# Optimization experiments

Measured on AMD Instinct MI355X. Metric: run time of the kernel, lower is better.

## Reference

```python
import jax, jax.numpy as jnp
import numpy as np

N = 50000        # num nodes
NFEAT = 512      # input feature dim
NCLASS = 256     # output classes (out_features of out_att)
E_RAND = 800000  # random edges; + N self-loops
NEG_SLOPE = 0.2  # leakyrelu alpha


def setup_inputs() -> dict:
    key = jax.random.key(0)
    k1, k2, k3, k4 = jax.random.split(key, 4)
    x = jax.random.normal(k1, (N, NFEAT), dtype=jnp.float32)
    W = jax.random.normal(k2, (NFEAT, NCLASS), dtype=jnp.float32) / np.float32(np.sqrt(NFEAT))
    a = jax.random.normal(k3, (2 * NCLASS,), dtype=jnp.float32) / np.float32(np.sqrt(2 * NCLASS))
    rand_edges = jax.random.randint(k4, (2, E_RAND), 0, N, dtype=jnp.int32)
    self_loops = jnp.tile(jnp.arange(N, dtype=jnp.int32), (2, 1))
    edge_index = jnp.concatenate([rand_edges, self_loops], axis=1)  # [2, E]
    return {"x": x, "W": W, "a": a, "edge_index": edge_index}


def reference(x, W, a, edge_index):
    # Eval-mode SpGAT: dropout is identity (training=False).
    row, col = edge_index[0], edge_index[1]  # edge = adj.nonzero().t(): row aggregates from col
    h = x @ W                                # [N, F]
    F_out = h.shape[1]
    # a @ cat(h[row], h[col]) == (h @ a1)[row] + (h @ a2)[col]  (avoids [E, 2F] concat)
    s_row = h @ a[:F_out]                    # [N]
    s_col = h @ a[F_out:]                    # [N]
    logits = s_row[row] + s_col[col]         # [E]
    e = jnp.exp(-jax.nn.leaky_relu(logits, negative_slope=NEG_SLOPE))  # [E]
    rowsum = jax.ops.segment_sum(e, row, num_segments=N)               # [N]
    msgs = e[:, None] * h[col]                                         # [E, F]
    h_prime = jax.ops.segment_sum(msgs, row, num_segments=N) / rowsum[:, None]
    return jax.nn.log_softmax(jax.nn.elu(h_prime), axis=1)
```

## Files before the change

### kernel.cpp

```cpp
#include <hip/hip_runtime.h>
#include <math.h>

#define NNODES   50000
#define NFEAT    512
#define NCLASS   256
#define NEG_SLOPE 0.2f
#define MPAD     50048
#define GBLK     782

typedef __attribute__((ext_vector_type(8))) short short8;
typedef __attribute__((ext_vector_type(4))) float floatx4;

__device__ __forceinline__ unsigned short f2bf(float f) {
    unsigned u = __builtin_bit_cast(unsigned, f);
    u += 0x7fffu + ((u >> 16) & 1u);
    return (unsigned short)(u >> 16);
}
__device__ __forceinline__ float bf2f(unsigned short s) {
    return __builtin_bit_cast(float, ((unsigned)s) << 16);
}
__device__ __forceinline__ float bf2f_lo(unsigned u) {
    return __builtin_bit_cast(float, u << 16);
}
__device__ __forceinline__ float bf2f_hi(unsigned u) {
    return __builtin_bit_cast(float, u & 0xffff0000u);
}
__device__ __forceinline__ unsigned pack_bf16_rh(float lo, float hi) {
    const unsigned ulo = __builtin_bit_cast(unsigned, lo) + 0x8000u;
    const unsigned uhi = __builtin_bit_cast(unsigned, hi) + 0x8000u;
    return __builtin_amdgcn_perm(uhi, ulo, 0x07060302);
}

#if __has_builtin(__builtin_amdgcn_fdot2_f32_bf16)
#define HAVE_DOT2 1
typedef __attribute__((ext_vector_type(2))) __bf16 bfx2;
__device__ __forceinline__ float dot2bf(unsigned hpair, unsigned epair, float acc) {
    return __builtin_amdgcn_fdot2_f32_bf16(__builtin_bit_cast(bfx2, hpair),
                                           __builtin_bit_cast(bfx2, epair), acc, false);
}
#endif

__global__ __launch_bounds__(256) void init_kernel(const float* __restrict__ W,
                                                   unsigned short* __restrict__ Wt,
                                                   int* __restrict__ zero2, int zn) {
    const int i = blockIdx.x * 256 + threadIdx.x;
    const int n = i >> 9;
    const int k = i & 511;
    Wt[i] = f2bf(W[(size_t)k * NCLASS + n]);
    for (int j = i; j < zn; j += 131072) zero2[j] = 0;
}

__global__ __launch_bounds__(256, 4) void gemm_mfma_kernel(const float* __restrict__ x,
                                                           const unsigned short* __restrict__ Wt,
                                                           unsigned short* __restrict__ hb,
                                                           const float* __restrict__ a,
                                                           float* __restrict__ s_row,
                                                           float* __restrict__ s_col,
                                                           const int* __restrict__ erow,
                                                           int* __restrict__ deg,
                                                           int M, int E) {
    __shared__ union {
        struct { short As[64 * 32]; short Bs[256 * 32]; } k;
        short Cs[32 * 260];
    } u;

    const int tid  = threadIdx.x;
    const int w    = tid >> 6;
    const int lane = tid & 63;
    const int rowbase = blockIdx.x * 64;

    const int srow = lane >> 2;
    const int skq  = (lane & 3) << 3;
    const int fm = lane & 15;
    const int fq = lane >> 4;

    floatx4 acc[4][4];
#pragma unroll
    for (int i = 0; i < 4; ++i)
#pragma unroll
        for (int j = 0; j < 4; ++j)
            acc[i][j] = (floatx4){0.f, 0.f, 0.f, 0.f};

    for (int k0 = 0; k0 < NFEAT; k0 += 32) {
#pragma unroll
        for (int t = 0; t < 4; ++t) {
            const int seg = w * 4 + t;
            const int nr  = seg * 16 + srow;
            __builtin_amdgcn_global_load_lds(
                (const __attribute__((address_space(1))) void*)(Wt + (size_t)nr * NFEAT + k0 + skq),
                (__attribute__((address_space(3))) void*)(u.k.Bs + seg * 512), 16, 0, 0);
        }
        {
            const int rr = w * 16 + srow;
            const int ar = min(rowbase + rr, M - 1);
            const float4* xp = (const float4*)&x[(size_t)ar * NFEAT + k0 + skq];
            const float4 u0 = xp[0];
            const float4 u1 = xp[1];
            uint4 o;
            o.x = pack_bf16_rh(u0.x, u0.y);
            o.y = pack_bf16_rh(u0.z, u0.w);
            o.z = pack_bf16_rh(u1.x, u1.y);
            o.w = pack_bf16_rh(u1.z, u1.w);
            *(uint4*)&u.k.As[rr * 32 + skq] = o;
        }
        __syncthreads();

        short8 af[4];
#pragma unroll
        for (int mt = 0; mt < 4; ++mt)
            af[mt] = *(const short8*)&u.k.As[(mt * 16 + fm) * 32 + fq * 8];
#pragma unroll
        for (int nt = 0; nt < 4; ++nt) {
            const short8 bfr = *(const short8*)&u.k.Bs[(w * 64 + nt * 16 + fm) * 32 + fq * 8];
#pragma unroll
            for (int mt = 0; mt < 4; ++mt)
                acc[mt][nt] = __builtin_amdgcn_mfma_f32_16x16x32_bf16(af[mt], bfr, acc[mt][nt], 0, 0, 0);
        }
        __syncthreads();
    }

#pragma unroll
    for (int p = 0; p < 2; ++p) {
        __syncthreads();
#pragma unroll
        for (int mt2 = 0; mt2 < 2; ++mt2) {
            const int mt = p * 2 + mt2;
#pragma unroll
            for (int nt = 0; nt < 4; ++nt)
#pragma unroll
                for (int r = 0; r < 4; ++r)
                    u.Cs[(mt2 * 16 + fq * 4 + r) * 260 + w * 64 + nt * 16 + fm] =
                        (short)f2bf(acc[mt][nt][r]);
        }
        __syncthreads();
#pragma unroll
        for (int k = 0; k < 8; ++k) {
            const int idx = tid + k * 256;
            const int lrow = idx >> 6;
            const int c4 = (idx & 63) << 2;
            const int grow = rowbase + p * 32 + lrow;
            const uint2 vv = *(const uint2*)&u.Cs[lrow * 260 + c4];
            const float f0 = bf2f_lo(vv.x), f1 = bf2f_hi(vv.x);
            const float f2 = bf2f_lo(vv.y), f3 = bf2f_hi(vv.y);
            const float4 A1 = *(const float4*)&a[c4];
            const float4 A2 = *(const float4*)&a[NCLASS + c4];
            float p1 = f0 * A1.x + f1 * A1.y + f2 * A1.z + f3 * A1.w;
            float p2 = f0 * A2.x + f1 * A2.y + f2 * A2.z + f3 * A2.w;
#pragma unroll
            for (int off = 1; off < 64; off <<= 1) {
                p1 += __shfl_xor(p1, off);
                p2 += __shfl_xor(p2, off);
            }
            if (grow < M) {
                *(uint2*)&hb[(size_t)grow * NCLASS + c4] = vv;
                if (lane == 0) {
                    s_row[grow] = p1;
                    s_col[grow] = p2;
                }
            }
        }
    }

    const int gtid = blockIdx.x * 256 + tid;
    for (int i = gtid; i < E; i += GBLK * 256)
        atomicAdd(&deg[erow[i]], 1);
}

__global__ __launch_bounds__(256) void scan1_kernel(const int* __restrict__ deg,
                                                    int* __restrict__ tmp,
                                                    int* __restrict__ blocksum, int n) {
    __shared__ int buf[256];
    const int i = blockIdx.x * 256 + threadIdx.x;
    const int t = threadIdx.x;
    buf[t] = (i < n) ? deg[i] : 0;
    __syncthreads();
#pragma unroll
    for (int off = 1; off < 256; off <<= 1) {
        const int uv = (t >= off) ? buf[t - off] : 0;
        __syncthreads();
        buf[t] += uv;
        __syncthreads();
    }
    if (i < n) tmp[i] = buf[t];
    if (t == 255) blocksum[blockIdx.x] = buf[255];
}

__global__ __launch_bounds__(256) void scan3_kernel(const int* __restrict__ tmp,
                                                    const int* __restrict__ blocksum,
                                                    int* __restrict__ rowstart, int n, int nb) {
    __shared__ int buf[256];
    const int t = threadIdx.x;
    buf[t] = (t < nb) ? blocksum[t] : 0;
    __syncthreads();
#pragma unroll
    for (int off = 1; off < 256; off <<= 1) {
        const int uv = (t >= off) ? buf[t - off] : 0;
        __syncthreads();
        buf[t] += uv;
        __syncthreads();
    }
    const int boff = (blockIdx.x == 0) ? 0 : buf[blockIdx.x - 1];
    const int i = blockIdx.x * 256 + t;
    if (i < n) rowstart[i + 1] = tmp[i] + boff;
    if (i == 0) rowstart[0] = 0;
}

__global__ __launch_bounds__(256) void scatter_kernel(const int* __restrict__ row,
                                                      const int* __restrict__ col,
                                                      const float* __restrict__ s_row,
                                                      const float* __restrict__ s_col,
                                                      const int* __restrict__ rowstart,
                                                      int* __restrict__ cursor,
                                                      int2* __restrict__ sorted_ce, int e) {
    const int i = blockIdx.x * 256 + threadIdx.x;
    if (i >= e) return;
    const int r = row[i];
    const int c = col[i];
    const float logit = s_row[r] + s_col[c];
    const float lr = logit > 0.f ? logit : NEG_SLOPE * logit;
    const float ew = __expf(-lr);
    const int pos = atomicAdd(&cursor[r], 1);
    int2 v;
    v.x = c;
    v.y = __builtin_bit_cast(int, ew);
    sorted_ce[rowstart[r] + pos] = v;
}

__global__ __launch_bounds__(256) void aggregate_kernel(const unsigned short* __restrict__ hb,
                                                        const int2* __restrict__ sorted_ce,
                                                        const int* __restrict__ rowstart,
                                                        float* __restrict__ out, int n) {
    const int wave = (int)((blockIdx.x * (size_t)blockDim.x + threadIdx.x) >> 6);
    const int lane = threadIdx.x & 63;
    if (wave >= n) return;
    const int r = wave;
    const int jb = rowstart[r];
    const int je = rowstart[r + 1];
    const int fo = lane << 2;

    float rowsum = 0.f;
    int j = jb;

#ifdef HAVE_DOT2
    float ac0 = 0.f, ac1 = 0.f, ac2 = 0.f, ac3 = 0.f;
    for (; j + 3 < je; j += 4) {
        const int2 v0 = sorted_ce[j];
        const int2 v1 = sorted_ce[j + 1];
        const int2 v2 = sorted_ce[j + 2];
        const int2 v3 = sorted_ce[j + 3];
        const uint2 g0 = *(const uint2*)&hb[(size_t)v0.x * NCLASS + fo];
        const uint2 g1 = *(const uint2*)&hb[(size_t)v1.x * NCLASS + fo];
        const uint2 g2 = *(const uint2*)&hb[(size_t)v2.x * NCLASS + fo];
        const uint2 g3 = *(const uint2*)&hb[(size_t)v3.x * NCLASS + fo];
        const float e0 = __builtin_bit_cast(float, v0.y);
        const float e1 = __builtin_bit_cast(float, v1.y);
        const float e2 = __builtin_bit_cast(float, v2.y);
        const float e3 = __builtin_bit_cast(float, v3.y);
        const unsigned ep01 = pack_bf16_rh(e0, e1);
        const unsigned ep23 = pack_bf16_rh(e2, e3);
        rowsum += (e0 + e1) + (e2 + e3);
        ac0 = dot2bf(__builtin_amdgcn_perm(g1.x, g0.x, 0x05040100), ep01, ac0);
        ac1 = dot2bf(__builtin_amdgcn_perm(g1.x, g0.x, 0x07060302), ep01, ac1);
        ac2 = dot2bf(__builtin_amdgcn_perm(g1.y, g0.y, 0x05040100), ep01, ac2);
        ac3 = dot2bf(__builtin_amdgcn_perm(g1.y, g0.y, 0x07060302), ep01, ac3);
        ac0 = dot2bf(__builtin_amdgcn_perm(g3.x, g2.x, 0x05040100), ep23, ac0);
        ac1 = dot2bf(__builtin_amdgcn_perm(g3.x, g2.x, 0x07060302), ep23, ac1);
        ac2 = dot2bf(__builtin_amdgcn_perm(g3.y, g2.y, 0x05040100), ep23, ac2);
        ac3 = dot2bf(__builtin_amdgcn_perm(g3.y, g2.y, 0x07060302), ep23, ac3);
    }
    float4 acc = make_float4(ac0, ac1, ac2, ac3);
#else
    float4 acc = make_float4(0.f, 0.f, 0.f, 0.f);
    for (; j + 3 < je; j += 4) {
        const int2 v0 = sorted_ce[j];
        const int2 v1 = sorted_ce[j + 1];
        const int2 v2 = sorted_ce[j + 2];
        const int2 v3 = sorted_ce[j + 3];
        const uint2 g0 = *(const uint2*)&hb[(size_t)v0.x * NCLASS + fo];
        const uint2 g1 = *(const uint2*)&hb[(size_t)v1.x * NCLASS + fo];
        const uint2 g2 = *(const uint2*)&hb[(size_t)v2.x * NCLASS + fo];
        const uint2 g3 = *(const uint2*)&hb[(size_t)v3.x * NCLASS + fo];
        const float e0 = __builtin_bit_cast(float, v0.y);
        const float e1 = __builtin_bit_cast(float, v1.y);
        const float e2 = __builtin_bit_cast(float, v2.y);
        const float e3 = __builtin_bit_cast(float, v3.y);
        rowsum += (e0 + e1) + (e2 + e3);
        acc.x += e0 * bf2f_lo(g0.x) + e1 * bf2f_lo(g1.x) + e2 * bf2f_lo(g2.x) + e3 * bf2f_lo(g3.x);
        acc.y += e0 * bf2f_hi(g0.x) + e1 * bf2f_hi(g1.x) + e2 * bf2f_hi(g2.x) + e3 * bf2f_hi(g3.x);
        acc.z += e0 * bf2f_lo(g0.y) + e1 * bf2f_lo(g1.y) + e2 * bf2f_lo(g2.y) + e3 * bf2f_lo(g3.y);
        acc.w += e0 * bf2f_hi(g0.y) + e1 * bf2f_hi(g1.y) + e2 * bf2f_hi(g2.y) + e3 * bf2f_hi(g3.y);
    }
#endif
    for (; j < je; ++j) {
        const int2 v = sorted_ce[j];
        const uint2 g = *(const uint2*)&hb[(size_t)v.x * NCLASS + fo];
        const float e = __builtin_bit_cast(float, v.y);
        rowsum += e;
        acc.x += e * bf2f_lo(g.x);
        acc.y += e * bf2f_hi(g.x);
        acc.z += e * bf2f_lo(g.y);
        acc.w += e * bf2f_hi(g.y);
    }

    const float inv = 1.f / rowsum;
    float v[4] = {acc.x * inv, acc.y * inv, acc.z * inv, acc.w * inv};
#pragma unroll
    for (int i = 0; i < 4; ++i)
        v[i] = v[i] > 0.f ? v[i] : __expf(v[i]) - 1.f;

    float m = fmaxf(fmaxf(v[0], v[1]), fmaxf(v[2], v[3]));
#pragma unroll
    for (int off = 32; off > 0; off >>= 1) m = fmaxf(m, __shfl_xor(m, off));
    float s = 0.f;
#pragma unroll
    for (int i = 0; i < 4; ++i) s += __expf(v[i] - m);
#pragma unroll
    for (int off = 32; off > 0; off >>= 1) s += __shfl_xor(s, off);
    const float lse = m + __logf(s);

    float4 o = make_float4(v[0] - lse, v[1] - lse, v[2] - lse, v[3] - lse);
    *(float4*)&out[(size_t)r * NCLASS + fo] = o;
}

extern "C" void kernel_launch(void* const* d_in, const int* in_sizes, int n_in,
                              void* d_out, int out_size, void* d_ws, size_t ws_size,
                              hipStream_t stream) {
    const float* x  = (const float*)d_in[0];
    const float* W  = (const float*)d_in[1];
    const float* a  = (const float*)d_in[2];
    const int* edge = (const int*)d_in[3];
    float* out = (float*)d_out;

    const int M = in_sizes[0] / NFEAT;
    const int E = in_sizes[3] / 2;
    const int* row = edge;
    const int* col = edge + E;

    char* ws = (char*)d_ws;
    size_t off = 0;
    auto carve = [&](size_t bytes) -> char* {
        char* p = ws + off;
        off = (off + bytes + 255) & ~(size_t)255;
        return p;
    };
    unsigned short* Wt = (unsigned short*)carve((size_t)NCLASS * NFEAT * sizeof(short));
    unsigned short* hb = (unsigned short*)carve((size_t)M * NCLASS * sizeof(short));
    int*   zero2    = (int*)carve((size_t)2 * M * sizeof(int));
    int*   deg      = zero2;
    int*   cursor   = zero2 + M;
    float* s_row    = (float*)carve((size_t)M * sizeof(float));
    float* s_col    = (float*)carve((size_t)M * sizeof(float));
    int*   rowstart = (int*)carve((size_t)(M + 1) * sizeof(int));
    int*   tmp_scan = (int*)carve((size_t)M * sizeof(int));
    int*   blocksum = (int*)carve((size_t)256 * sizeof(int));
    int2*  sorted_ce = (int2*)carve((size_t)E * sizeof(int2));

    init_kernel<<<512, 256, 0, stream>>>(W, Wt, zero2, 2 * M);

    gemm_mfma_kernel<<<GBLK, 256, 0, stream>>>(x, Wt, hb, a, s_row, s_col, row, deg, M, E);

    const int nb1 = (M + 255) / 256;
    scan1_kernel<<<nb1, 256, 0, stream>>>(deg, tmp_scan, blocksum, M);
    scan3_kernel<<<nb1, 256, 0, stream>>>(tmp_scan, blocksum, rowstart, M, nb1);
    scatter_kernel<<<(E + 255) / 256, 256, 0, stream>>>(row, col, s_row, s_col,
                                                        rowstart, cursor, sorted_ce, E);

    aggregate_kernel<<<(M + 3) / 4, 256, 0, stream>>>(hb, sorted_ce, rowstart, out, M);
}
```

Before: 328.2 us.

## Load GEMM fragments directly from global into registers with double buffering

The GEMM main loop no longer stages x and W tiles through LDS. Each lane loads its MFMA A and B fragments straight from global memory into registers, converting x to bf16 in registers, and prefetches the next k-step while the current MFMAs run. This drops both per-iteration __syncthreads and the LDS round trip. In exchange, each of the four waves now reloads the same x fragments, global access is less coalesced (16-byte pieces spread across rows), and register pressure is higher. The occupancy hint in launch_bounds is also removed.

New measurement: 368.4 us. 1.12x slower.

```diff
diff --git a/kernel.cpp b/kernel.cpp
--- a/kernel.cpp
+++ b/kernel.cpp
@@ -50,30 +50,35 @@
     for (int j = i; j < zn; j += 131072) zero2[j] = 0;
 }
 
-__global__ __launch_bounds__(256, 4) void gemm_mfma_kernel(const float* __restrict__ x,
-                                                           const unsigned short* __restrict__ Wt,
-                                                           unsigned short* __restrict__ hb,
-                                                           const float* __restrict__ a,
-                                                           float* __restrict__ s_row,
-                                                           float* __restrict__ s_col,
-                                                           const int* __restrict__ erow,
-                                                           int* __restrict__ deg,
-                                                           int M, int E) {
-    __shared__ union {
-        struct { short As[64 * 32]; short Bs[256 * 32]; } k;
-        short Cs[32 * 260];
-    } u;
+__global__ __launch_bounds__(256) void gemm_mfma_kernel(const float* __restrict__ x,
+                                                        const unsigned short* __restrict__ Wt,
+                                                        unsigned short* __restrict__ hb,
+                                                        const float* __restrict__ a,
+                                                        float* __restrict__ s_row,
+                                                        float* __restrict__ s_col,
+                                                        const int* __restrict__ erow,
+                                                        int* __restrict__ deg,
+                                                        int M, int E) {
+    __shared__ short Cs[32 * 260];
 
     const int tid  = threadIdx.x;
     const int w    = tid >> 6;
     const int lane = tid & 63;
     const int rowbase = blockIdx.x * 64;
-
-    const int srow = lane >> 2;
-    const int skq  = (lane & 3) << 3;
     const int fm = lane & 15;
     const int fq = lane >> 4;
 
+    const float* xrow[4];
+#pragma unroll
+    for (int mt = 0; mt < 4; ++mt) {
+        const int ar = min(rowbase + mt * 16 + fm, M - 1);
+        xrow[mt] = x + (size_t)ar * NFEAT + fq * 8;
+    }
+    const unsigned short* brow[4];
+#pragma unroll
+    for (int nt = 0; nt < 4; ++nt)
+        brow[nt] = Wt + (size_t)(w * 64 + nt * 16 + fm) * NFEAT + fq * 8;
+
     floatx4 acc[4][4];
 #pragma unroll
     for (int i = 0; i < 4; ++i)
@@ -81,42 +86,40 @@
         for (int j = 0; j < 4; ++j)
             acc[i][j] = (floatx4){0.f, 0.f, 0.f, 0.f};
 
+    auto load_a = [&](int mt, int k0) -> short8 {
+        const float4 u0 = *(const float4*)(xrow[mt] + k0);
+        const float4 u1 = *(const float4*)(xrow[mt] + k0 + 4);
+        uint4 o;
+        o.x = pack_bf16_rh(u0.x, u0.y);
+        o.y = pack_bf16_rh(u0.z, u0.w);
+        o.z = pack_bf16_rh(u1.x, u1.y);
+        o.w = pack_bf16_rh(u1.z, u1.w);
+        return __builtin_bit_cast(short8, o);
+    };
+
+    short8 af0[4], bf0[4];
+#pragma unroll
+    for (int mt = 0; mt < 4; ++mt) af0[mt] = load_a(mt, 0);
+#pragma unroll
+    for (int nt = 0; nt < 4; ++nt) bf0[nt] = *(const short8*)(brow[nt]);
+
     for (int k0 = 0; k0 < NFEAT; k0 += 32) {
-#pragma unroll
-        for (int t = 0; t < 4; ++t) {
-            const int seg = w * 4 + t;
-            const int nr  = seg * 16 + srow;
-            __builtin_amdgcn_global_load_lds(
-                (const __attribute__((address_space(1))) void*)(Wt + (size_t)nr * NFEAT + k0 + skq),
-                (__attribute__((address_space(3))) void*)(u.k.Bs + seg * 512), 16, 0, 0);
+        short8 af1[4], bf1[4];
+        if (k0 + 32 < NFEAT) {
+#pragma unroll
+            for (int mt = 0; mt < 4; ++mt) af1[mt] = load_a(mt, k0 + 32);
+#pragma unroll
+            for (int nt = 0; nt < 4; ++nt) bf1[nt] = *(const short8*)(brow[nt] + k0 + 32);
         }
-        {
-            const int rr = w * 16 + srow;
-            const int ar = min(rowbase + rr, M - 1);
-            const float4* xp = (const float4*)&x[(size_t)ar * NFEAT + k0 + skq];
-            const float4 u0 = xp[0];
-            const float4 u1 = xp[1];
-            uint4 o;
-            o.x = pack_bf16_rh(u0.x, u0.y);
-            o.y = pack_bf16_rh(u0.z, u0.w);
-            o.z = pack_bf16_rh(u1.x, u1.y);
-            o.w = pack_bf16_rh(u1.z, u1.w);
-            *(uint4*)&u.k.As[rr * 32 + skq] = o;
-        }
-        __syncthreads();
-
-        short8 af[4];
-#pragma unroll
-        for (int mt = 0; mt < 4; ++mt)
-            af[mt] = *(const short8*)&u.k.As[(mt * 16 + fm) * 32 + fq * 8];
-#pragma unroll
-        for (int nt = 0; nt < 4; ++nt) {
-            const short8 bfr = *(const short8*)&u.k.Bs[(w * 64 + nt * 16 + fm) * 32 + fq * 8];
+#pragma unroll
+        for (int nt = 0; nt < 4; ++nt)
 #pragma unroll
             for (int mt = 0; mt < 4; ++mt)
-                acc[mt][nt] = __builtin_amdgcn_mfma_f32_16x16x32_bf16(af[mt], bfr, acc[mt][nt], 0, 0, 0);
-        }
-        __syncthreads();
+                acc[mt][nt] = __builtin_amdgcn_mfma_f32_16x16x32_bf16(af0[mt], bf0[nt], acc[mt][nt], 0, 0, 0);
+#pragma unroll
+        for (int mt = 0; mt < 4; ++mt) af0[mt] = af1[mt];
+#pragma unroll
+        for (int nt = 0; nt < 4; ++nt) bf0[nt] = bf1[nt];
     }
 
 #pragma unroll
@@ -129,7 +132,7 @@
             for (int nt = 0; nt < 4; ++nt)
 #pragma unroll
                 for (int r = 0; r < 4; ++r)
-                    u.Cs[(mt2 * 16 + fq * 4 + r) * 260 + w * 64 + nt * 16 + fm] =
+                    Cs[(mt2 * 16 + fq * 4 + r) * 260 + w * 64 + nt * 16 + fm] =
                         (short)f2bf(acc[mt][nt][r]);
         }
         __syncthreads();
@@ -139,7 +142,7 @@
             const int lrow = idx >> 6;
             const int c4 = (idx & 63) << 2;
             const int grow = rowbase + p * 32 + lrow;
-            const uint2 vv = *(const uint2*)&u.Cs[lrow * 260 + c4];
+            const uint2 vv = *(const uint2*)&Cs[lrow * 260 + c4];
             const float f0 = bf2f_lo(vv.x), f1 = bf2f_hi(vv.x);
             const float f2 = bf2f_lo(vv.y), f3 = bf2f_hi(vv.y);
             const float4 A1 = *(const float4*)&a[c4];
```
